# Performance work log

Hardware: AMD Instinct MI355X
Metric: run time of the kernel (lower is better)

Reference implementation:

```python
import jax, jax.numpy as jnp
import numpy as np

KS = 3                 # kernel_size
DILATIONS = (1, 2, 3)  # dilation list
NUM_HEADS = 6


def _unfold_reflect(x, ks, dil):
    """ReflectionPad2d(dil*(ks-1)//2) + Unfold(ks, dilation=dil).
    x: [B, C, H, W] -> [B, C*ks*ks, H, W] (channel-major like torch Unfold)."""
    pad = dil * (ks - 1) // 2
    xp = jnp.pad(x, ((0, 0), (0, 0), (pad, pad), (pad, pad)), mode='reflect')
    return jax.lax.conv_general_dilated_patches(
        xp, filter_shape=(ks, ks), window_strides=(1, 1), padding='VALID',
        rhs_dilation=(dil, dil))  # [B, C*ks*ks, H, W]


def _dilate_attention(q, k, v, head_dim, ks, dil):
    """q,k,v: [B, c2, H, W] -> [B, H, W, c2]."""
    B, c2, H, W = q.shape
    nh = c2 // head_dim
    scale = head_dim ** (-0.5)
    P = H * W
    k2 = ks * ks
    # q -> [B, nh, P, hd]
    qr = q.reshape(B, nh, head_dim, P).transpose(0, 1, 3, 2)
    # unfold k, v -> [B, c2*k2, H, W], channel order (c, kh, kw)
    ku = _unfold_reflect(k, ks, dil).reshape(B, nh, head_dim, k2, P)
    vu = _unfold_reflect(v, ks, dil).reshape(B, nh, head_dim, k2, P)
    kr = ku.transpose(0, 1, 4, 2, 3)  # [B, nh, P, hd, k2]
    vr = vu.transpose(0, 1, 4, 3, 2)  # [B, nh, P, k2, hd]
    scores = jnp.einsum('bnpd,bnpdk->bnpk', qr, kr) * scale
    attn = jax.nn.softmax(scores, axis=-1)
    out = jnp.einsum('bnpk,bnpkd->bnpd', attn, vr)  # [B, nh, P, hd]
    return out.transpose(0, 2, 1, 3).reshape(B, H, W, nh * head_dim)


def _forward(x, pos_w, pos_b, qkv_w, proj_w):
    B, C, H, W = x.shape
    nd = len(DILATIONS)
    c2 = C // nd
    head_dim = C // NUM_HEADS
    # depthwise 3x3 positional conv (groups=C) + residual
    pe = jax.lax.conv_general_dilated(
        x, pos_w, window_strides=(1, 1), padding=((1, 1), (1, 1)),
        dimension_numbers=('NCHW', 'OIHW', 'NCHW'), feature_group_count=C)
    x = x + pe + pos_b[None, :, None, None]
    # 1x1 qkv conv
    qkv = jnp.einsum('oc,bchw->bohw', qkv_w, x)  # [B, 3C, H, W]
    # 'b (three nd c2) h w -> nd three b c2 h w'
    qkv = qkv.reshape(B, 3, nd, c2, H, W).transpose(2, 1, 0, 3, 4, 5)
    outs = []
    for i, dil in enumerate(DILATIONS):
        o = _dilate_attention(qkv[i, 0], qkv[i, 1], qkv[i, 2], head_dim, KS, dil)
        outs.append(o.transpose(0, 3, 1, 2))  # [B, c2, H, W]
    xo = jnp.concatenate(outs, axis=1)  # [B, C, H, W], dilation-major channels
    return jnp.einsum('oc,bchw->bohw', proj_w, xo)


def setup_inputs() -> dict:
    key = jax.random.key(0)
    ks = jax.random.split(key, 5)
    B, C, H, W = 4, 192, 128, 128
    return {
        'x': jax.random.normal(ks[0], (B, C, H, W), dtype=jnp.float32),
        'pos_w': jax.random.normal(ks[1], (C, 1, 3, 3), dtype=jnp.float32) * 0.05,
        'pos_b': jax.random.normal(ks[2], (C,), dtype=jnp.float32) * 0.05,
        'qkv_w': jax.random.normal(ks[3], (3 * C, C), dtype=jnp.float32) * (C ** -0.5),
        'proj_w': jax.random.normal(ks[4], (C, C), dtype=jnp.float32) * (C ** -0.5),
    }


def reference(x, pos_w, pos_b, qkv_w, proj_w):
    return _forward(x, pos_w, pos_b, qkv_w, proj_w)
```

## Files before the change

### kernel.cpp

```cpp
#include <hip/hip_runtime.h>
#include <hip/hip_bf16.h>
#include <math.h>

#define Hdim 128
#define Wdim 128
#define HW   16384
#define Cdim 192
#define Bdim 4
#define QKVC 576
#define NTOT (Bdim * HW)

typedef __attribute__((ext_vector_type(8))) short short8;
typedef __attribute__((ext_vector_type(4))) short short4v;
typedef __attribute__((ext_vector_type(4))) float f32x4;

__device__ __forceinline__ void async_ld16(void* lds, const void* g) {
    __builtin_amdgcn_global_load_lds(
        (const __attribute__((address_space(1))) void*)g,
        (__attribute__((address_space(3))) void*)lds, 16, 0, 0);
}
__device__ __forceinline__ float lo16(unsigned u) { return __uint_as_float(u << 16); }
__device__ __forceinline__ float hi16(unsigned u) { return __uint_as_float(u & 0xffff0000u); }

__global__ void convert_w(const float* __restrict__ qkv_w,
                          const float* __restrict__ proj_w,
                          __hip_bfloat16* __restrict__ Wq,
                          __hip_bfloat16* __restrict__ Wp) {
    int i = blockIdx.x * 256 + threadIdx.x;
    if (i < QKVC * Cdim) {
        Wq[i] = __float2bfloat16(qkv_w[i]);
    } else {
        int j = i - QKVC * Cdim;
        Wp[j] = __float2bfloat16(proj_w[j]);
    }
}

__global__ __launch_bounds__(256, 5)
void posconv_nhwc(const float* __restrict__ x,
                  const float* __restrict__ pos_w,
                  const float* __restrict__ pos_b,
                  __hip_bfloat16* __restrict__ Xb) {
    __shared__ __align__(16) float xs[3 * 16 * 128];
    __shared__ __hip_bfloat16 tile[16][132];

    int t = threadIdx.x;
    int id = blockIdx.x;
    int xj = id & 7;
    int r_ = id >> 3;
    int rb = r_ & 15;
    int cg = (r_ >> 4) % 12;
    int b  = (r_ >> 4) / 12;
    int h  = xj * 16 + rb;

    int hm = h > 0 ? h - 1 : 0;
    int hp = h < Hdim - 1 ? h + 1 : Hdim - 1;
    int hh0 = hm, hh1 = h, hh2 = hp;

    int ch = t >> 4;
    int qh = t & 15;
    int cglob = cg * 16 + ch;

    const float* wp = pos_w + cglob * 9;
    float w0 = wp[0], w1 = wp[1], w2 = wp[2];
    float w3 = wp[3], w4 = wp[4], w5 = wp[5];
    float w6 = wp[6], w7 = wp[7], w8 = wp[8];
    float bias = pos_b[cglob];
    float m0 = (h > 0) ? 1.f : 0.f;
    float m2 = (h < Hdim - 1) ? 1.f : 0.f;
    w0 *= m0; w1 *= m0; w2 *= m0;
    w6 *= m2; w7 *= m2; w8 *= m2;

    {
        const float* xg = x + (size_t)(b * Cdim + cg * 16) * HW;
#pragma unroll
        for (int k = 0; k < 6; ++k) {
            int u = t + k * 256;
            int rowi = u >> 5;
            int ql = u & 31;
            int rr = rowi >> 4;
            int sch = rowi & 15;
            int hr = rr == 0 ? hh0 : (rr == 1 ? hh1 : hh2);
            int qs = ql ^ sch;
            async_ld16((char*)xs + (size_t)u * 16,
                       xg + (size_t)sch * HW + hr * Wdim + qs * 4);
        }
    }
    __syncthreads();

    float out[8];
    const char* xsb = (const char*)xs;
#pragma unroll
    for (int rr = 0; rr < 3; ++rr) {
        const char* rowb = xsb + (size_t)(rr * 16 + ch) * 512;
        float4 lo = *(const float4*)(rowb + (((2 * qh)     ^ ch) * 16));
        float4 hi = *(const float4*)(rowb + (((2 * qh + 1) ^ ch) * 16));
        float L = __shfl_up(hi.w, 1, 64);
        float R = __shfl_down(lo.x, 1, 64);
        if (qh == 0)  L = 0.f;
        if (qh == 15) R = 0.f;
        float v0 = L,    v1 = lo.x, v2 = lo.y, v3 = lo.z, v4 = lo.w;
        float v5 = hi.x, v6 = hi.y, v7 = hi.z, v8 = hi.w, v9 = R;
        float wa, wb, wc;
        if (rr == 0)      { wa = w0; wb = w1; wc = w2; }
        else if (rr == 1) { wa = w3; wb = w4; wc = w5; }
        else              { wa = w6; wb = w7; wc = w8; }
        if (rr == 1) {
            out[0] = v1 + bias; out[1] = v2 + bias; out[2] = v3 + bias;
            out[3] = v4 + bias; out[4] = v5 + bias; out[5] = v6 + bias;
            out[6] = v7 + bias; out[7] = v8 + bias;
        }
        if (rr == 0) {
            out[0] = wa * v0 + wb * v1 + wc * v2;
            out[1] = wa * v1 + wb * v2 + wc * v3;
            out[2] = wa * v2 + wb * v3 + wc * v4;
            out[3] = wa * v3 + wb * v4 + wc * v5;
            out[4] = wa * v4 + wb * v5 + wc * v6;
            out[5] = wa * v5 + wb * v6 + wc * v7;
            out[6] = wa * v6 + wb * v7 + wc * v8;
            out[7] = wa * v7 + wb * v8 + wc * v9;
        } else if (rr == 1) {
            out[0] += wa * v0 + wb * v1 + wc * v2;
            out[1] += wa * v1 + wb * v2 + wc * v3;
            out[2] += wa * v2 + wb * v3 + wc * v4;
            out[3] += wa * v3 + wb * v4 + wc * v5;
            out[4] += wa * v4 + wb * v5 + wc * v6;
            out[5] += wa * v5 + wb * v6 + wc * v7;
            out[6] += wa * v6 + wb * v7 + wc * v8;
            out[7] += wa * v7 + wb * v8 + wc * v9;
        } else {
            out[0] += wa * v0 + wb * v1 + wc * v2;
            out[1] += wa * v1 + wb * v2 + wc * v3;
            out[2] += wa * v2 + wb * v3 + wc * v4;
            out[3] += wa * v3 + wb * v4 + wc * v5;
            out[4] += wa * v4 + wb * v5 + wc * v6;
            out[5] += wa * v5 + wb * v6 + wc * v7;
            out[6] += wa * v6 + wb * v7 + wc * v8;
            out[7] += wa * v7 + wb * v8 + wc * v9;
        }
    }


    {
        const char* r0b = xsb + (size_t)(0 * 16 + ch) * 512;
        const char* r1b = xsb + (size_t)(1 * 16 + ch) * 512;
        const char* r2b = xsb + (size_t)(2 * 16 + ch) * 512;
        float4 lo0 = *(const float4*)(r0b + (((2 * qh)     ^ ch) * 16));
        float4 hi0 = *(const float4*)(r0b + (((2 * qh + 1) ^ ch) * 16));
        float4 lo1 = *(const float4*)(r1b + (((2 * qh)     ^ ch) * 16));
        float4 hi1 = *(const float4*)(r1b + (((2 * qh + 1) ^ ch) * 16));
        float4 lo2 = *(const float4*)(r2b + (((2 * qh)     ^ ch) * 16));
        float4 hi2 = *(const float4*)(r2b + (((2 * qh + 1) ^ ch) * 16));
        float L0 = __shfl_up(hi0.w, 1, 64), R0 = __shfl_down(lo0.x, 1, 64);
        float L1 = __shfl_up(hi1.w, 1, 64), R1 = __shfl_down(lo1.x, 1, 64);
        float L2 = __shfl_up(hi2.w, 1, 64), R2 = __shfl_down(lo2.x, 1, 64);
        if (qh == 0)  { L0 = 0.f; L1 = 0.f; L2 = 0.f; }
        if (qh == 15) { R0 = 0.f; R1 = 0.f; R2 = 0.f; }
        float a0[10] = {L0, lo0.x, lo0.y, lo0.z, lo0.w, hi0.x, hi0.y, hi0.z, hi0.w, R0};
        float a1[10] = {L1, lo1.x, lo1.y, lo1.z, lo1.w, hi1.x, hi1.y, hi1.z, hi1.w, R1};
        float a2[10] = {L2, lo2.x, lo2.y, lo2.z, lo2.w, hi2.x, hi2.y, hi2.z, hi2.w, R2};
#pragma unroll
        for (int i = 0; i < 8; ++i) {
            out[i] = a1[i + 1] + bias
                   + w0 * a0[i] + w1 * a0[i + 1] + w2 * a0[i + 2]
                   + w3 * a1[i] + w4 * a1[i + 1] + w5 * a1[i + 2]
                   + w6 * a2[i] + w7 * a2[i + 1] + w8 * a2[i + 2];
        }
    }

    union { unsigned short u[8]; short8 v; } pk;
#pragma unroll
    for (int i = 0; i < 8; ++i) {
        __hip_bfloat16 bv = __float2bfloat16(out[i]);
        pk.u[i] = *(unsigned short*)&bv;
    }
    *(short8*)(void*)&tile[ch][qh * 8] = pk.v;
    __syncthreads();

    int px = t >> 1, s2 = t & 1;
    union { unsigned short u[8]; short8 v; } o;
#pragma unroll
    for (int j = 0; j < 8; ++j)
        o.u[j] = *(const unsigned short*)&tile[s2 * 8 + j][px];
    size_t p0img = (size_t)(b << 14) + (size_t)h * Wdim;
    *(short8*)(void*)(Xb + (p0img + px) * Cdim + cg * 16 + s2 * 8) = o.v;
}

template <int MODE, int MT>
__global__ __launch_bounds__(256, 2)
void gemm_mfma(const __hip_bfloat16* __restrict__ Wb,
               const __hip_bfloat16* __restrict__ Xt,
               void* __restrict__ Cout) {
    __shared__ __hip_bfloat16 As[64 * 32];
    __shared__ __hip_bfloat16 Bs[256 * 32];
    const int t = threadIdx.x;
    const int w = t >> 6, l = t & 63;
    const int lq = l >> 4, lr = l & 15;
    const int id = blockIdx.x;
    const int xj = id & 7;
    const int rest = id >> 3;
    const int m0 = (rest % MT) * 64;
    const int n0 = ((rest / MT) * 8 + xj) * 256;

    f32x4 acc[4][4] = {};

    for (int kt = 0; kt < 6; ++kt) {
        const int k0 = kt * 32;
        {
            int m = t >> 2, kc = t & 3;
            async_ld16(As + t * 8, Wb + (size_t)(m0 + m) * Cdim + k0 + kc * 8);
        }
#pragma unroll
        for (int it = 0; it < 4; ++it) {
            int idx = it * 256 + t;
            int n = idx >> 2, kc = idx & 3;
            const __hip_bfloat16* src;
            if (MODE == 0)
                src = Xt + (size_t)(n0 + n) * Cdim + k0 + kc * 8;
            else
                src = Xt + (size_t)kt * ((size_t)NTOT * 32) +
                      (size_t)(n0 + n) * 32 + kc * 8;
            async_ld16(Bs + idx * 8, src);
        }
        __syncthreads();

        short8 af[4], bf[4];
#pragma unroll
        for (int i = 0; i < 4; ++i)
            af[i] = *(const short8*)(void*)(As + (i * 16 + lr) * 32 + lq * 8);
#pragma unroll
        for (int j = 0; j < 4; ++j)
            bf[j] = *(const short8*)(void*)(Bs + (w * 64 + j * 16 + lr) * 32 + lq * 8);
#pragma unroll
        for (int i = 0; i < 4; ++i)
#pragma unroll
            for (int j = 0; j < 4; ++j)
                acc[i][j] = __builtin_amdgcn_mfma_f32_16x16x32_bf16(
                    af[i], bf[j], acc[i][j], 0, 0, 0);
        __syncthreads();
    }

#pragma unroll
    for (int i = 0; i < 4; ++i) {
        int mb = m0 + i * 16 + lq * 4;
#pragma unroll
        for (int j = 0; j < 4; ++j) {
            int n = n0 + w * 64 + j * 16 + lr;
            if (MODE == 0) {
                int three = mb / 192, rem = mb % 192;
                int pi = rem >> 6, pn = (rem >> 5) & 1, d4 = rem & 31;
                size_t plane = (size_t)((three * 3 + pi) * 2 + pn);
                __hip_bfloat16* dst = (__hip_bfloat16*)Cout +
                    plane * ((size_t)NTOT * 32) + (size_t)n * 32 + d4;
                short4v pk;
#pragma unroll
                for (int r = 0; r < 4; ++r) {
                    __hip_bfloat16 bv = __float2bfloat16(acc[i][j][r]);
                    pk[r] = *(short*)&bv;
                }
                *(short4v*)(void*)dst = pk;
            } else {
                int b = n >> 14, p = n & (HW - 1);
#pragma unroll
                for (int r = 0; r < 4; ++r)
                    ((float*)Cout)[((size_t)(b * Cdim + mb + r)) * HW + p] =
                        acc[i][j][r];
            }
        }
    }
}

__global__ __launch_bounds__(256, 3)
void attn_kernel(const __hip_bfloat16* __restrict__ QKV,
                 __hip_bfloat16* __restrict__ AO) {
    __shared__ __align__(16) unsigned char lds[6][8192];

    int t = threadIdx.x;
    int pix = t >> 1, s = t & 1;
    int id = blockIdx.x;
    int xj = id & 7;
    int rest = id >> 3;
    int cb = rest >> 4;
    int k16 = rest & 15;
    int h = xj * 16 + k16;
    int b = cb / 6, comb = cb % 6;
    int dil = (comb >> 1) + 1;

    int w = pix;
    int col = (b << 14) + h * Wdim + w;

    const size_t PS = (size_t)NTOT * 32;
    const __hip_bfloat16* Qp = QKV + (size_t)comb * PS;
    const __hip_bfloat16* Kp = Qp + 6 * PS;
    const __hip_bfloat16* Vp = Qp + 12 * PS;

    const uint4* qp = (const uint4*)(Qp + (size_t)col * 32) + s * 2;
    uint4 qv0 = qp[0], qv1 = qp[1];

    int hh[3];
#pragma unroll
    for (int kh = 0; kh < 3; ++kh) {
        int v = h + (kh - 1) * dil;
        hh[kh] = v < 0 ? -v : (v >= Hdim ? 2 * Hdim - 2 - v : v);
    }
    int j0 = t, j1 = t + 256;
    int g0 = j0 ^ ((j0 >> 3) & 7);
    int g1 = j1 ^ ((j1 >> 3) & 7);
#pragma unroll
    for (int r = 0; r < 3; ++r) {
        size_t rowe = ((size_t)(b << 14) + (size_t)hh[r] * Wdim) * 32;
        async_ld16(&lds[r][j0 * 16],     Kp + rowe + g0 * 8);
        async_ld16(&lds[r][j1 * 16],     Kp + rowe + g1 * 8);
        async_ld16(&lds[r + 3][j0 * 16], Vp + rowe + g0 * 8);
        async_ld16(&lds[r + 3][j1 * 16], Vp + rowe + g1 * 8);
    }
    __syncthreads();

    float q[16];
    {
        uint4 x = qv0;
        q[0] = lo16(x.x); q[1] = hi16(x.x);
        q[2] = lo16(x.y); q[3] = hi16(x.y);
        q[4] = lo16(x.z); q[5] = hi16(x.z);
        q[6] = lo16(x.w); q[7] = hi16(x.w);
        x = qv1;
        q[8]  = lo16(x.x); q[9]  = hi16(x.x);
        q[10] = lo16(x.y); q[11] = hi16(x.y);
        q[12] = lo16(x.z); q[13] = hi16(x.z);
        q[14] = lo16(x.w); q[15] = hi16(x.w);
    }

    int coff[3];
#pragma unroll
    for (int kw = 0; kw < 3; ++kw) {
        int ww = w + (kw - 1) * dil;
        ww = ww < 0 ? -ww : (ww >= Wdim ? 2 * Wdim - 2 - ww : ww);
        int i0 = 4 * ww + 2 * s;
        coff[kw] = (i0 ^ ((ww >> 1) & 7)) * 16;
    }

    float sc[9];
#pragma unroll
    for (int kh = 0; kh < 3; ++kh)
#pragma unroll
        for (int kw = 0; kw < 3; ++kw) {
            uint4 xa = *(const uint4*)(void*)&lds[kh][coff[kw]];
            uint4 xb = *(const uint4*)(void*)&lds[kh][coff[kw] ^ 16];
            float p0 = 0.f;
            p0 += q[0] * lo16(xa.x) + q[1] * hi16(xa.x);
            p0 += q[2] * lo16(xa.y) + q[3] * hi16(xa.y);
            p0 += q[4] * lo16(xa.z) + q[5] * hi16(xa.z);
            p0 += q[6] * lo16(xa.w) + q[7] * hi16(xa.w);
            p0 += q[8]  * lo16(xb.x) + q[9]  * hi16(xb.x);
            p0 += q[10] * lo16(xb.y) + q[11] * hi16(xb.y);
            p0 += q[12] * lo16(xb.z) + q[13] * hi16(xb.z);
            p0 += q[14] * lo16(xb.w) + q[15] * hi16(xb.w);
            sc[kh * 3 + kw] = p0;
        }

#pragma unroll
    for (int j = 0; j < 9; ++j)
        sc[j] = (sc[j] + __shfl_xor(sc[j], 1, 64)) * 0.17677669529663687f;

    float m = sc[0];
#pragma unroll
    for (int j = 1; j < 9; ++j) m = fmaxf(m, sc[j]);
    float sum = 0.f;
#pragma unroll
    for (int j = 0; j < 9; ++j) { sc[j] = __expf(sc[j] - m); sum += sc[j]; }
    float inv = 1.f / sum;

    float acc[16] = {};
#pragma unroll
    for (int kh = 0; kh < 3; ++kh)
#pragma unroll
        for (int kw = 0; kw < 3; ++kw) {
            float a = sc[kh * 3 + kw];
            uint4 xa = *(const uint4*)(void*)&lds[kh + 3][coff[kw]];
            uint4 xb = *(const uint4*)(void*)&lds[kh + 3][coff[kw] ^ 16];
            acc[0] += a * lo16(xa.x); acc[1] += a * hi16(xa.x);
            acc[2] += a * lo16(xa.y); acc[3] += a * hi16(xa.y);
            acc[4] += a * lo16(xa.z); acc[5] += a * hi16(xa.z);
            acc[6] += a * lo16(xa.w); acc[7] += a * hi16(xa.w);
            acc[8]  += a * lo16(xb.x); acc[9]  += a * hi16(xb.x);
            acc[10] += a * lo16(xb.y); acc[11] += a * hi16(xb.y);
            acc[12] += a * lo16(xb.z); acc[13] += a * hi16(xb.z);
            acc[14] += a * lo16(xb.w); acc[15] += a * hi16(xb.w);
        }

    union { unsigned short hu[16]; short8 v[2]; } o;
#pragma unroll
    for (int d = 0; d < 16; ++d) {
        __hip_bfloat16 bv = __float2bfloat16(acc[d] * inv);
        o.hu[d] = *(unsigned short*)&bv;
    }
    short8* dst = (short8*)(void*)(AO + (size_t)comb * PS + (size_t)col * 32 + s * 16);
#pragma unroll
    for (int u = 0; u < 2; ++u) dst[u] = o.v[u];
}

extern "C" void kernel_launch(void* const* d_in, const int* in_sizes, int n_in,
                              void* d_out, int out_size, void* d_ws, size_t ws_size,
                              hipStream_t stream) {
    const float* x      = (const float*)d_in[0];
    const float* pos_w  = (const float*)d_in[1];
    const float* pos_b  = (const float*)d_in[2];
    const float* qkv_w  = (const float*)d_in[3];
    const float* proj_w = (const float*)d_in[4];
    float* out = (float*)d_out;

    char* ws = (char*)d_ws;
    __hip_bfloat16* Xb  = (__hip_bfloat16*)ws;
    __hip_bfloat16* QKV = (__hip_bfloat16*)(ws + (size_t)25165824);
    __hip_bfloat16* AO  = (__hip_bfloat16*)(ws + (size_t)100663296);
    __hip_bfloat16* Wq  = (__hip_bfloat16*)(ws + (size_t)125829120);
    __hip_bfloat16* Wp  = (__hip_bfloat16*)(ws + (size_t)126050304);

    convert_w<<<(QKVC * Cdim + Cdim * Cdim) / 256, 256, 0, stream>>>(
        qkv_w, proj_w, Wq, Wp);

    posconv_nhwc<<<6144, 256, 0, stream>>>(x, pos_w, pos_b, Xb);

    gemm_mfma<0, 9><<<2304, 256, 0, stream>>>(Wq, Xb, QKV);

    attn_kernel<<<3072, 256, 0, stream>>>(QKV, AO);

    gemm_mfma<1, 3><<<768, 256, 0, stream>>>(Wp, AO, out);
}
```

Measured before the change: 187.4 us.

## Double-buffer MFMA GEMM LDS tiles and drop duplicated posconv stencil pass

The bf16 MFMA GEMM now keeps two LDS buffers per operand and issues the async global-to-LDS loads for the next K slice before computing on the current one. This removes one barrier per K step and overlaps load latency with MFMA work. The launch-bounds occupancy hint rises from 2 to 3 blocks to go with it. The positional-conv kernel loses a first stencil loop whose results were recomputed by the block that follows, cutting redundant LDS reads and FMAs at the cost of doubled GEMM LDS footprint.

```diff
diff --git a/kernel.cpp b/kernel.cpp
--- a/kernel.cpp
+++ b/kernel.cpp
@@ -52,9 +52,9 @@
     int b  = (r_ >> 4) / 12;
     int h  = xj * 16 + rb;
 
-    int hm = h > 0 ? h - 1 : 0;
-    int hp = h < Hdim - 1 ? h + 1 : Hdim - 1;
-    int hh0 = hm, hh1 = h, hh2 = hp;
+    int hh0 = h > 0 ? h - 1 : 0;
+    int hh1 = h;
+    int hh2 = h < Hdim - 1 ? h + 1 : Hdim - 1;
 
     int ch = t >> 4;
     int qh = t & 15;
@@ -88,59 +88,8 @@
     __syncthreads();
 
     float out[8];
-    const char* xsb = (const char*)xs;
-#pragma unroll
-    for (int rr = 0; rr < 3; ++rr) {
-        const char* rowb = xsb + (size_t)(rr * 16 + ch) * 512;
-        float4 lo = *(const float4*)(rowb + (((2 * qh)     ^ ch) * 16));
-        float4 hi = *(const float4*)(rowb + (((2 * qh + 1) ^ ch) * 16));
-        float L = __shfl_up(hi.w, 1, 64);
-        float R = __shfl_down(lo.x, 1, 64);
-        if (qh == 0)  L = 0.f;
-        if (qh == 15) R = 0.f;
-        float v0 = L,    v1 = lo.x, v2 = lo.y, v3 = lo.z, v4 = lo.w;
-        float v5 = hi.x, v6 = hi.y, v7 = hi.z, v8 = hi.w, v9 = R;
-        float wa, wb, wc;
-        if (rr == 0)      { wa = w0; wb = w1; wc = w2; }
-        else if (rr == 1) { wa = w3; wb = w4; wc = w5; }
-        else              { wa = w6; wb = w7; wc = w8; }
-        if (rr == 1) {
-            out[0] = v1 + bias; out[1] = v2 + bias; out[2] = v3 + bias;
-            out[3] = v4 + bias; out[4] = v5 + bias; out[5] = v6 + bias;
-            out[6] = v7 + bias; out[7] = v8 + bias;
-        }
-        if (rr == 0) {
-            out[0] = wa * v0 + wb * v1 + wc * v2;
-            out[1] = wa * v1 + wb * v2 + wc * v3;
-            out[2] = wa * v2 + wb * v3 + wc * v4;
-            out[3] = wa * v3 + wb * v4 + wc * v5;
-            out[4] = wa * v4 + wb * v5 + wc * v6;
-            out[5] = wa * v5 + wb * v6 + wc * v7;
-            out[6] = wa * v6 + wb * v7 + wc * v8;
-            out[7] = wa * v7 + wb * v8 + wc * v9;
-        } else if (rr == 1) {
-            out[0] += wa * v0 + wb * v1 + wc * v2;
-            out[1] += wa * v1 + wb * v2 + wc * v3;
-            out[2] += wa * v2 + wb * v3 + wc * v4;
-            out[3] += wa * v3 + wb * v4 + wc * v5;
-            out[4] += wa * v4 + wb * v5 + wc * v6;
-            out[5] += wa * v5 + wb * v6 + wc * v7;
-            out[6] += wa * v6 + wb * v7 + wc * v8;
-            out[7] += wa * v7 + wb * v8 + wc * v9;
-        } else {
-            out[0] += wa * v0 + wb * v1 + wc * v2;
-            out[1] += wa * v1 + wb * v2 + wc * v3;
-            out[2] += wa * v2 + wb * v3 + wc * v4;
-            out[3] += wa * v3 + wb * v4 + wc * v5;
-            out[4] += wa * v4 + wb * v5 + wc * v6;
-            out[5] += wa * v5 + wb * v6 + wc * v7;
-            out[6] += wa * v6 + wb * v7 + wc * v8;
-            out[7] += wa * v7 + wb * v8 + wc * v9;
-        }
-    }
-
-
     {
+        const char* xsb = (const char*)xs;
         const char* r0b = xsb + (size_t)(0 * 16 + ch) * 512;
         const char* r1b = xsb + (size_t)(1 * 16 + ch) * 512;
         const char* r2b = xsb + (size_t)(2 * 16 + ch) * 512;
@@ -186,12 +135,12 @@
 }
 
 template <int MODE, int MT>
-__global__ __launch_bounds__(256, 2)
+__global__ __launch_bounds__(256, 3)
 void gemm_mfma(const __hip_bfloat16* __restrict__ Wb,
                const __hip_bfloat16* __restrict__ Xt,
                void* __restrict__ Cout) {
-    __shared__ __hip_bfloat16 As[64 * 32];
-    __shared__ __hip_bfloat16 Bs[256 * 32];
+    __shared__ __hip_bfloat16 As[2][64 * 32];
+    __shared__ __hip_bfloat16 Bs[2][256 * 32];
     const int t = threadIdx.x;
     const int w = t >> 6, l = t & 63;
     const int lq = l >> 4, lr = l & 15;
@@ -201,41 +150,50 @@
     const int m0 = (rest % MT) * 64;
     const int n0 = ((rest / MT) * 8 + xj) * 256;
 
-    f32x4 acc[4][4] = {};
-
-    for (int kt = 0; kt < 6; ++kt) {
-        const int k0 = kt * 32;
-        {
-            int m = t >> 2, kc = t & 3;
-            async_ld16(As + t * 8, Wb + (size_t)(m0 + m) * Cdim + k0 + kc * 8);
-        }
+    const int ms = t >> 2, kcs = t & 3;
+
+    auto stage = [&](int buf, int kt_) {
+        const int k0_ = kt_ * 32;
+        async_ld16(As[buf] + t * 8,
+                   Wb + (size_t)(m0 + ms) * Cdim + k0_ + kcs * 8);
 #pragma unroll
         for (int it = 0; it < 4; ++it) {
             int idx = it * 256 + t;
             int n = idx >> 2, kc = idx & 3;
             const __hip_bfloat16* src;
             if (MODE == 0)
-                src = Xt + (size_t)(n0 + n) * Cdim + k0 + kc * 8;
+                src = Xt + (size_t)(n0 + n) * Cdim + k0_ + kc * 8;
             else
-                src = Xt + (size_t)kt * ((size_t)NTOT * 32) +
+                src = Xt + (size_t)kt_ * ((size_t)NTOT * 32) +
                       (size_t)(n0 + n) * 32 + kc * 8;
-            async_ld16(Bs + idx * 8, src);
-        }
-        __syncthreads();
+            async_ld16(Bs[buf] + idx * 8, src);
+        }
+    };
+
+    f32x4 acc[4][4] = {};
+
+    stage(0, 0);
+    __syncthreads();
+
+#pragma unroll
+    for (int kt = 0; kt < 6; ++kt) {
+        const int cur = kt & 1;
+        if (kt < 5) stage(cur ^ 1, kt + 1);
 
         short8 af[4], bf[4];
 #pragma unroll
         for (int i = 0; i < 4; ++i)
-            af[i] = *(const short8*)(void*)(As + (i * 16 + lr) * 32 + lq * 8);
+            af[i] = *(const short8*)(void*)(As[cur] + (i * 16 + lr) * 32 + lq * 8);
 #pragma unroll
         for (int j = 0; j < 4; ++j)
-            bf[j] = *(const short8*)(void*)(Bs + (w * 64 + j * 16 + lr) * 32 + lq * 8);
+            bf[j] = *(const short8*)(void*)(Bs[cur] + (w * 64 + j * 16 + lr) * 32 + lq * 8);
 #pragma unroll
         for (int i = 0; i < 4; ++i)
 #pragma unroll
             for (int j = 0; j < 4; ++j)
                 acc[i][j] = __builtin_amdgcn_mfma_f32_16x16x32_bf16(
                     af[i], bf[j], acc[i][j], 0, 0, 0);
+
         __syncthreads();
     }
 
```

After: 188.6 us. Within noise of the previous version (+0.6%).
